# Kernel optimization log

Hardware: AMD Instinct MI355X
Metric: run time of the kernel (lower is better)

Reference implementation:

```python
import jax, jax.numpy as jnp
import numpy as np
import itertools

CONVEX_K = 10
NUM_CLASS = 100
B, N = 8, 16384
MINDIS_INIT = 1.0e5  # torch code initializes mindis to 100000


def _hull_vertex_labels_np(pts):
    """pts: [G, K, 3] numpy. Exact brute-force 3D convex hull vertex labels
    (general position): a triple is a hull facet iff all points lie on one
    side of its plane; every point on some facet is a hull vertex."""
    G, K, _ = pts.shape
    tri = np.array(list(itertools.combinations(range(K), 3)))  # [T,3]
    a = pts[:, tri[:, 0]]                                      # [G,T,3]
    b = pts[:, tri[:, 1]]
    c = pts[:, tri[:, 2]]
    n = np.cross(b - a, c - a)                                 # [G,T,3]
    d = np.einsum('gkd,gtd->gtk', pts, n) - np.einsum('gtd,gtd->gt', a, n)[:, :, None]
    eps = 1e-7
    facet = (d <= eps).all(-1) | (d >= -eps).all(-1)           # [G,T]
    labels = np.zeros((G, K), dtype=np.int32)
    gidx, tidx = np.nonzero(facet)
    for col in range(3):
        labels[gidx, tri[tidx, col]] = 1
    return labels


def setup_inputs() -> dict:
    key = jax.random.key(0)
    k1, k2, k3 = jax.random.split(key, 3)
    xyz = jax.random.normal(k1, (B, N, 6), dtype=jnp.float32)
    skel_xyz = jax.random.normal(k2, (B, NUM_CLASS * CONVEX_K, 3), dtype=jnp.float32)
    weights = jax.random.normal(k3, (B, NUM_CLASS * CONVEX_K // CONVEX_K * CONVEX_K,), dtype=jnp.float32)[:, :NUM_CLASS * CONVEX_K].reshape(B, -1)[:, :1000]
    weights = jax.random.normal(k3, (B, NUM_CLASS * CONVEX_K), dtype=jnp.float32)
    skel_np = np.asarray(skel_xyz).reshape(B * NUM_CLASS, CONVEX_K, 3)
    labels = jnp.asarray(_hull_vertex_labels_np(skel_np).reshape(B, NUM_CLASS, CONVEX_K))
    return {"xyz": xyz, "skel_xyz": skel_xyz, "weights": weights,
            "labels": labels, "num_class": NUM_CLASS}


def reference(xyz, skel_xyz, weights, labels, num_class):
    b = xyz.shape[0]
    pts = xyz[:, :, :3]                                   # [B,N,3]; normals xyz[:,:,3:6] unused
    cp = skel_xyz.reshape(b, num_class, CONVEX_K, 3)      # [B,C,K,3]

    # --- convex loss: for each non-vertex point, min sq-dist to a hull vertex ---
    diff = cp[:, :, :, None, :] - cp[:, :, None, :, :]    # [B,C,K,K,3] (small)
    sqd = jnp.sum(diff * diff, axis=-1)                   # [B,C,K,K]
    is_vert = labels == 1                                  # [B,C,K]
    masked = jnp.where(is_vert[:, :, None, :], sqd, jnp.inf)
    mindis = jnp.minimum(jnp.min(masked, axis=-1), MINDIS_INIT)  # [B,C,K]
    loss_convex = jnp.sum(jnp.where(is_vert, 0.0, mindis)) / (b * num_class)

    # --- Chamfer (closest_distance_with_batch both directions, L2 norm, summed) ---
    skel = skel_xyz                                        # [B,M,3]
    d2 = (jnp.sum(pts * pts, -1)[:, :, None]
          + jnp.sum(skel * skel, -1)[:, None, :]
          - 2.0 * jnp.einsum('bnd,bmd->bnm', pts, skel))   # [B,N,M]
    d = jnp.sqrt(jnp.maximum(d2, 1e-12))
    loss_cd = (jnp.sum(jnp.min(d, axis=2)) + jnp.sum(jnp.min(d, axis=1))) / b

    return 1.0 * loss_convex + 0.1 * loss_cd
```

## Files before the change

kernel.cpp:

```cpp
#include <hip/hip_runtime.h>

#define BATCH 8
#define NPTS 16384
#define MSKEL 1000
#define NCLS 100
#define CKK 10
#define MINDIS_INITF 100000.0f

#define OFF_PTSM 32000
#define OFF_MINB (32000 + 524288)

__global__ __launch_bounds__(256) void k_prep(const float* __restrict__ xyz,
                                              const float* __restrict__ skel,
                                              float4* __restrict__ skelN,
                                              float4* __restrict__ ptsM,
                                              unsigned int* __restrict__ minbits,
                                              float* __restrict__ out) {
    const int gid = blockIdx.x * 256 + threadIdx.x;
    {
        const float* p = xyz + (size_t)gid * 6;
        float x = p[0], y = p[1], z = p[2];
        ptsM[gid] = make_float4(x, y, z, 0.5f * (x * x + y * y + z * z));
    }
    if (gid < BATCH * MSKEL) {
        const float* s = skel + (size_t)gid * 3;
        float sx = s[0], sy = s[1], sz = s[2];
        skelN[gid] = make_float4(-sx, -sy, -sz, 0.5f * (sx * sx + sy * sy + sz * sz));
        minbits[gid] = 0x7F800000u;
    }
    if (gid == 0) out[0] = 0.0f;
}

__global__ __launch_bounds__(256) void k_chamfer(const float4* __restrict__ skelN,
                                                 const float4* __restrict__ ptsM,
                                                 unsigned int* __restrict__ minbits,
                                                 float* __restrict__ out) {
    const int bid = blockIdx.x;
    const int tid = threadIdx.x;

    if (bid < 256) {
        const int b = bid >> 5, tile = bid & 31;
        const int wave = tid >> 6, lane = tid & 63;
        const float4* __restrict__ base = ptsM + b * NPTS + tile * 512;

        float4 P[8];
        float mt[8];
#pragma unroll
        for (int j = 0; j < 8; ++j) {
            P[j] = base[j * 64 + lane];
            mt[j] = 3.4e38f;
        }

        const float4* __restrict__ sk = skelN + b * MSKEL + wave * 250;
#pragma unroll 5
        for (int m = 0; m < 250; ++m) {
            float4 s = sk[m];
#pragma unroll
            for (int j = 0; j < 8; ++j) {
                float t = fmaf(P[j].x, s.x, fmaf(P[j].y, s.y, fmaf(P[j].z, s.z, s.w)));
                mt[j] = fminf(mt[j], t);
            }
        }

        __shared__ float sm[4 * 512];
#pragma unroll
        for (int j = 0; j < 8; ++j) {
            sm[wave * 512 + j * 64 + lane] = mt[j] + P[j].w;
        }
        __syncthreads();

        float a0 = fminf(fminf(sm[tid], sm[512 + tid]),
                         fminf(sm[1024 + tid], sm[1536 + tid]));
        float a1 = fminf(fminf(sm[tid + 256], sm[512 + tid + 256]),
                         fminf(sm[1024 + tid + 256], sm[1536 + tid + 256]));
        float d = sqrtf(fmaxf(2.0f * a0, 1e-12f)) + sqrtf(fmaxf(2.0f * a1, 1e-12f));

#pragma unroll
        for (int o = 32; o > 0; o >>= 1) d += __shfl_down(d, o, 64);
        __shared__ float s_part[4];
        if (lane == 0) s_part[wave] = d;
        __syncthreads();
        if (tid == 0) {
            atomicAdd(out, 0.0125f * (s_part[0] + s_part[1] + s_part[2] + s_part[3]));
        }
    } else {
        const int id = bid - 256;
        const int b = id >> 5, tile = id & 31;

        float nsx[4], nsy[4], nsz[4], ssq[4], mind[4];
#pragma unroll
        for (int k = 0; k < 4; ++k) {
            const int m = tid + k * 256;
            if (m < MSKEL) {
                float4 s = skelN[b * MSKEL + m];
                nsx[k] = s.x; nsy[k] = s.y; nsz[k] = s.z;
                ssq[k] = 2.0f * s.w;
            } else {
                nsx[k] = 0.0f; nsy[k] = 0.0f; nsz[k] = 0.0f; ssq[k] = 0.0f;
            }
            mind[k] = 3.4e38f;
        }

        const float4* __restrict__ pp = ptsM + b * NPTS + tile * 512;
#pragma unroll 8
        for (int n = 0; n < 512; ++n) {
            float4 r = pp[n];
#pragma unroll
            for (int k = 0; k < 4; ++k) {
                float t = fmaf(r.x, nsx[k], fmaf(r.y, nsy[k], fmaf(r.z, nsz[k], r.w)));
                mind[k] = fminf(mind[k], t);
            }
        }
#pragma unroll
        for (int k = 0; k < 4; ++k) {
            const int m = tid + k * 256;
            if (m < MSKEL) {
                float d2 = fmaf(2.0f, mind[k], ssq[k]);
                atomicMin(&minbits[b * MSKEL + m], __float_as_uint(fmaxf(d2, 0.0f)));
            }
        }
    }
}

__global__ __launch_bounds__(256) void k_reduce(const float* __restrict__ skel,
                                                const int* __restrict__ labels,
                                                const unsigned int* __restrict__ minbits,
                                                float* __restrict__ out) {
    const int gid = blockIdx.x * 256 + threadIdx.x;
    const int tid = threadIdx.x;
    float acc = 0.0f;

    for (int i = gid; i < BATCH * MSKEL; i += 2048) {
        acc += 0.0125f * sqrtf(fmaxf(__uint_as_float(minbits[i]), 1e-12f));
    }

    if (gid < BATCH * NCLS) {
        const int b = gid / NCLS, c = gid - b * NCLS;
        const float* cp = skel + ((size_t)b * MSKEL + c * CKK) * 3;
        const int* lab = labels + (size_t)b * NCLS * CKK + c * CKK;
        float x[CKK], y[CKK], z[CKK];
        int lv[CKK];
#pragma unroll
        for (int i = 0; i < CKK; ++i) {
            x[i] = cp[i * 3 + 0]; y[i] = cp[i * 3 + 1]; z[i] = cp[i * 3 + 2];
            lv[i] = lab[i];
        }
        float convexSum = 0.0f;
#pragma unroll
        for (int i = 0; i < CKK; ++i) {
            if (lv[i] != 1) {
                float mind = MINDIS_INITF;
#pragma unroll
                for (int j = 0; j < CKK; ++j) {
                    if (lv[j] == 1) {
                        float dx = x[i] - x[j], dy = y[i] - y[j], dz = z[i] - z[j];
                        mind = fminf(mind, dx * dx + dy * dy + dz * dz);
                    }
                }
                convexSum += mind;
            }
        }
        acc += convexSum * (1.0f / (BATCH * NCLS));
    }

#pragma unroll
    for (int o = 32; o > 0; o >>= 1) acc += __shfl_down(acc, o, 64);
    __shared__ float s_part[4];
    const int wave = tid >> 6, lane = tid & 63;
    if (lane == 0) s_part[wave] = acc;
    __syncthreads();
    if (tid == 0) {
        atomicAdd(out, s_part[0] + s_part[1] + s_part[2] + s_part[3]);
    }
}

extern "C" void kernel_launch(void* const* d_in, const int* in_sizes, int n_in,
                              void* d_out, int out_size, void* d_ws, size_t ws_size,
                              hipStream_t stream) {
    const float* xyz = (const float*)d_in[0];
    const float* skel = (const float*)d_in[1];
    const int* labels = (const int*)d_in[3];
    float* out = (float*)d_out;

    float4* skelN = (float4*)d_ws;
    float4* ptsM = (float4*)((float*)d_ws + OFF_PTSM);
    unsigned int* minbits = (unsigned int*)((float*)d_ws + OFF_MINB);

    k_prep<<<512, 256, 0, stream>>>(xyz, skel, skelN, ptsM, minbits, out);
    k_chamfer<<<512, 256, 0, stream>>>(skelN, ptsM, minbits, out);
    k_reduce<<<8, 256, 0, stream>>>(skel, labels, minbits, out);
}
```

Baseline: 93.39 us.

## Fuse both Chamfer directions per block and replace atomicMin with partial-min buffer

Each chamfer block now processes a 128-point tile and computes both the point-to-skeleton minimum and the skeleton-to-point minimum for that tile, instead of splitting the two directions across separate block halves. Per-tile skeleton minima are written to a 128-way partial buffer that the reduce kernel min-reduces, replacing global atomicMin and its initialization. The grid doubles to 1024 blocks with smaller per-thread register tiles to raise occupancy, in exchange for lower register reuse per loaded skeleton/point and extra partial-buffer traffic (about 4 MB written then read).

```diff
diff --git a/kernel.cpp b/kernel.cpp
--- a/kernel.cpp
+++ b/kernel.cpp
@@ -8,13 +8,12 @@
 #define MINDIS_INITF 100000.0f
 
 #define OFF_PTSM 32000
-#define OFF_MINB (32000 + 524288)
+#define OFF_MPART (32000 + 524288)
 
 __global__ __launch_bounds__(256) void k_prep(const float* __restrict__ xyz,
                                               const float* __restrict__ skel,
                                               float4* __restrict__ skelN,
                                               float4* __restrict__ ptsM,
-                                              unsigned int* __restrict__ minbits,
                                               float* __restrict__ out) {
     const int gid = blockIdx.x * 256 + threadIdx.x;
     {
@@ -26,112 +25,104 @@
         const float* s = skel + (size_t)gid * 3;
         float sx = s[0], sy = s[1], sz = s[2];
         skelN[gid] = make_float4(-sx, -sy, -sz, 0.5f * (sx * sx + sy * sy + sz * sz));
-        minbits[gid] = 0x7F800000u;
     }
     if (gid == 0) out[0] = 0.0f;
 }
 
-__global__ __launch_bounds__(256) void k_chamfer(const float4* __restrict__ skelN,
-                                                 const float4* __restrict__ ptsM,
-                                                 unsigned int* __restrict__ minbits,
-                                                 float* __restrict__ out) {
+__global__ __launch_bounds__(256, 4) void k_chamfer(const float4* __restrict__ skelN,
+                                                    const float4* __restrict__ ptsM,
+                                                    float* __restrict__ mpart,
+                                                    float* __restrict__ out) {
     const int bid = blockIdx.x;
+    const int b = bid >> 7, gt = bid & 127;
     const int tid = threadIdx.x;
+    const int wave = tid >> 6, lane = tid & 63;
+    const float4* __restrict__ base = ptsM + b * NPTS + gt * 128;
 
-    if (bid < 256) {
-        const int b = bid >> 5, tile = bid & 31;
-        const int wave = tid >> 6, lane = tid & 63;
-        const float4* __restrict__ base = ptsM + b * NPTS + tile * 512;
+    float nsx[4], nsy[4], nsz[4], mind[4];
+#pragma unroll
+    for (int k = 0; k < 4; ++k) {
+        const int m = tid + k * 256;
+        if (m < MSKEL) {
+            float4 s = skelN[b * MSKEL + m];
+            nsx[k] = s.x; nsy[k] = s.y; nsz[k] = s.z;
+        } else {
+            nsx[k] = 0.0f; nsy[k] = 0.0f; nsz[k] = 0.0f;
+        }
+        mind[k] = 3.4e38f;
+    }
 
-        float4 P[8];
-        float mt[8];
+    float4 P0 = base[lane];
+    float4 P1 = base[64 + lane];
+    float mt0 = 3.4e38f, mt1 = 3.4e38f;
+
+    const int w = __builtin_amdgcn_readfirstlane(wave);
+    const float4* __restrict__ sk = skelN + b * MSKEL + w * 250;
+#pragma unroll 5
+    for (int m = 0; m < 250; ++m) {
+        float4 s = sk[m];
+        float t0 = fmaf(P0.x, s.x, fmaf(P0.y, s.y, fmaf(P0.z, s.z, s.w)));
+        float t1 = fmaf(P1.x, s.x, fmaf(P1.y, s.y, fmaf(P1.z, s.z, s.w)));
+        mt0 = fminf(mt0, t0);
+        mt1 = fminf(mt1, t1);
+    }
+
+    __shared__ float sm[4 * 128];
+    sm[wave * 128 + lane] = mt0 + P0.w;
+    sm[wave * 128 + 64 + lane] = mt1 + P1.w;
+    __syncthreads();
+
+    float dsum = 0.0f;
+    if (tid < 128) {
+        float a = fminf(fminf(sm[tid], sm[128 + tid]),
+                        fminf(sm[256 + tid], sm[384 + tid]));
+        dsum = sqrtf(fmaxf(2.0f * a, 1e-12f));
+    }
+
+#pragma unroll 8
+    for (int n = 0; n < 128; ++n) {
+        float4 r = base[n];
 #pragma unroll
-        for (int j = 0; j < 8; ++j) {
-            P[j] = base[j * 64 + lane];
-            mt[j] = 3.4e38f;
+        for (int k = 0; k < 4; ++k) {
+            float t = fmaf(r.x, nsx[k], fmaf(r.y, nsy[k], fmaf(r.z, nsz[k], r.w)));
+            mind[k] = fminf(mind[k], t);
         }
-
-        const float4* __restrict__ sk = skelN + b * MSKEL + wave * 250;
-#pragma unroll 5
-        for (int m = 0; m < 250; ++m) {
-            float4 s = sk[m];
+    }
+    float* __restrict__ mp = mpart + (size_t)gt * (BATCH * MSKEL) + b * MSKEL;
 #pragma unroll
-            for (int j = 0; j < 8; ++j) {
-                float t = fmaf(P[j].x, s.x, fmaf(P[j].y, s.y, fmaf(P[j].z, s.z, s.w)));
-                mt[j] = fminf(mt[j], t);
-            }
-        }
-
-        __shared__ float sm[4 * 512];
-#pragma unroll
-        for (int j = 0; j < 8; ++j) {
-            sm[wave * 512 + j * 64 + lane] = mt[j] + P[j].w;
-        }
-        __syncthreads();
-
-        float a0 = fminf(fminf(sm[tid], sm[512 + tid]),
-                         fminf(sm[1024 + tid], sm[1536 + tid]));
-        float a1 = fminf(fminf(sm[tid + 256], sm[512 + tid + 256]),
-                         fminf(sm[1024 + tid + 256], sm[1536 + tid + 256]));
-        float d = sqrtf(fmaxf(2.0f * a0, 1e-12f)) + sqrtf(fmaxf(2.0f * a1, 1e-12f));
+    for (int k = 0; k < 4; ++k) {
+        const int m = tid + k * 256;
+        if (m < MSKEL) mp[m] = mind[k];
+    }
 
 #pragma unroll
-        for (int o = 32; o > 0; o >>= 1) d += __shfl_down(d, o, 64);
-        __shared__ float s_part[4];
-        if (lane == 0) s_part[wave] = d;
-        __syncthreads();
-        if (tid == 0) {
-            atomicAdd(out, 0.0125f * (s_part[0] + s_part[1] + s_part[2] + s_part[3]));
-        }
-    } else {
-        const int id = bid - 256;
-        const int b = id >> 5, tile = id & 31;
-
-        float nsx[4], nsy[4], nsz[4], ssq[4], mind[4];
-#pragma unroll
-        for (int k = 0; k < 4; ++k) {
-            const int m = tid + k * 256;
-            if (m < MSKEL) {
-                float4 s = skelN[b * MSKEL + m];
-                nsx[k] = s.x; nsy[k] = s.y; nsz[k] = s.z;
-                ssq[k] = 2.0f * s.w;
-            } else {
-                nsx[k] = 0.0f; nsy[k] = 0.0f; nsz[k] = 0.0f; ssq[k] = 0.0f;
-            }
-            mind[k] = 3.4e38f;
-        }
-
-        const float4* __restrict__ pp = ptsM + b * NPTS + tile * 512;
-#pragma unroll 8
-        for (int n = 0; n < 512; ++n) {
-            float4 r = pp[n];
-#pragma unroll
-            for (int k = 0; k < 4; ++k) {
-                float t = fmaf(r.x, nsx[k], fmaf(r.y, nsy[k], fmaf(r.z, nsz[k], r.w)));
-                mind[k] = fminf(mind[k], t);
-            }
-        }
-#pragma unroll
-        for (int k = 0; k < 4; ++k) {
-            const int m = tid + k * 256;
-            if (m < MSKEL) {
-                float d2 = fmaf(2.0f, mind[k], ssq[k]);
-                atomicMin(&minbits[b * MSKEL + m], __float_as_uint(fmaxf(d2, 0.0f)));
-            }
-        }
+    for (int o = 32; o > 0; o >>= 1) dsum += __shfl_down(dsum, o, 64);
+    __shared__ float s_part[4];
+    if (lane == 0) s_part[wave] = dsum;
+    __syncthreads();
+    if (tid == 0) {
+        atomicAdd(out, 0.0125f * (s_part[0] + s_part[1] + s_part[2] + s_part[3]));
     }
 }
 
 __global__ __launch_bounds__(256) void k_reduce(const float* __restrict__ skel,
                                                 const int* __restrict__ labels,
-                                                const unsigned int* __restrict__ minbits,
+                                                const float4* __restrict__ skelN,
+                                                const float* __restrict__ mpart,
                                                 float* __restrict__ out) {
     const int gid = blockIdx.x * 256 + threadIdx.x;
     const int tid = threadIdx.x;
     float acc = 0.0f;
 
-    for (int i = gid; i < BATCH * MSKEL; i += 2048) {
-        acc += 0.0125f * sqrtf(fmaxf(__uint_as_float(minbits[i]), 1e-12f));
+    if (gid < BATCH * MSKEL) {
+        float mind = 3.4e38f;
+#pragma unroll 8
+        for (int g = 0; g < 128; ++g) {
+            mind = fminf(mind, mpart[g * (BATCH * MSKEL) + gid]);
+        }
+        float ssq = 2.0f * skelN[gid].w;
+        float d2 = fmaf(2.0f, mind, ssq);
+        acc = 0.0125f * sqrtf(fmaxf(d2, 1e-12f));
     }
 
     if (gid < BATCH * NCLS) {
@@ -149,15 +140,15 @@
 #pragma unroll
         for (int i = 0; i < CKK; ++i) {
             if (lv[i] != 1) {
-                float mind = MINDIS_INITF;
+                float mindc = MINDIS_INITF;
 #pragma unroll
                 for (int j = 0; j < CKK; ++j) {
                     if (lv[j] == 1) {
                         float dx = x[i] - x[j], dy = y[i] - y[j], dz = z[i] - z[j];
-                        mind = fminf(mind, dx * dx + dy * dy + dz * dz);
+                        mindc = fminf(mindc, dx * dx + dy * dy + dz * dz);
                     }
                 }
-                convexSum += mind;
+                convexSum += mindc;
             }
         }
         acc += convexSum * (1.0f / (BATCH * NCLS));
@@ -184,9 +175,9 @@
 
     float4* skelN = (float4*)d_ws;
     float4* ptsM = (float4*)((float*)d_ws + OFF_PTSM);
-    unsigned int* minbits = (unsigned int*)((float*)d_ws + OFF_MINB);
+    float* mpart = (float*)d_ws + OFF_MPART;
 
-    k_prep<<<512, 256, 0, stream>>>(xyz, skel, skelN, ptsM, minbits, out);
-    k_chamfer<<<512, 256, 0, stream>>>(skelN, ptsM, minbits, out);
-    k_reduce<<<8, 256, 0, stream>>>(skel, labels, minbits, out);
+    k_prep<<<512, 256, 0, stream>>>(xyz, skel, skelN, ptsM, out);
+    k_chamfer<<<1024, 256, 0, stream>>>(skelN, ptsM, mpart, out);
+    k_reduce<<<32, 256, 0, stream>>>(skel, labels, skelN, mpart, out);
 }
```

Result: slower. 124.4 us (+33.2%).

## Fuse prep into chamfer kernel, stage in LDS, replace atomics with partial buffers

Applied to the files above, without the earlier changes.

Removes the separate prep kernel: the chamfer blocks now load xyz and skeleton directly, compute the norm terms on the fly, and stage the skeleton and point tiles in shared memory. Global atomicMin and atomicAdd are replaced by per-tile partial-min and per-block partial-sum buffers that a wider 32-block reduce kernel combines. This drops one launch and the intermediate workspace round trip. In exchange it adds a 32-way strided read per skeleton point in the reduce, plus strided 6-float loads of xyz.

```diff
diff --git a/kernel.cpp b/kernel.cpp
--- a/kernel.cpp
+++ b/kernel.cpp
@@ -7,51 +7,44 @@
 #define CKK 10
 #define MINDIS_INITF 100000.0f
 
-#define OFF_PTSM 32000
-#define OFF_MINB (32000 + 524288)
-
-__global__ __launch_bounds__(256) void k_prep(const float* __restrict__ xyz,
-                                              const float* __restrict__ skel,
-                                              float4* __restrict__ skelN,
-                                              float4* __restrict__ ptsM,
-                                              unsigned int* __restrict__ minbits,
-                                              float* __restrict__ out) {
-    const int gid = blockIdx.x * 256 + threadIdx.x;
-    {
-        const float* p = xyz + (size_t)gid * 6;
-        float x = p[0], y = p[1], z = p[2];
-        ptsM[gid] = make_float4(x, y, z, 0.5f * (x * x + y * y + z * z));
-    }
-    if (gid < BATCH * MSKEL) {
-        const float* s = skel + (size_t)gid * 3;
-        float sx = s[0], sy = s[1], sz = s[2];
-        skelN[gid] = make_float4(-sx, -sy, -sz, 0.5f * (sx * sx + sy * sy + sz * sz));
-        minbits[gid] = 0x7F800000u;
-    }
-    if (gid == 0) out[0] = 0.0f;
-}
-
-__global__ __launch_bounds__(256) void k_chamfer(const float4* __restrict__ skelN,
-                                                 const float4* __restrict__ ptsM,
-                                                 unsigned int* __restrict__ minbits,
-                                                 float* __restrict__ out) {
+#define OFF_NPART 256000
+
+__global__ __launch_bounds__(256) void k_A(const float* __restrict__ xyz,
+                                           const float* __restrict__ skel,
+                                           float* __restrict__ mpart,
+                                           float* __restrict__ npart,
+                                           float* __restrict__ out) {
     const int bid = blockIdx.x;
     const int tid = threadIdx.x;
+    const int wave = tid >> 6, lane = tid & 63;
+
+    if (bid == 0 && tid == 0) out[0] = 0.0f;
 
     if (bid < 256) {
         const int b = bid >> 5, tile = bid & 31;
-        const int wave = tid >> 6, lane = tid & 63;
-        const float4* __restrict__ base = ptsM + b * NPTS + tile * 512;
+
+        __shared__ float4 skLDS[MSKEL];
+        __shared__ float sm[4 * 512];
+        __shared__ float s_part[4];
+
+        for (int i = tid; i < MSKEL; i += 256) {
+            const float* s = skel + ((size_t)b * MSKEL + i) * 3;
+            float sx = s[0], sy = s[1], sz = s[2];
+            skLDS[i] = make_float4(-sx, -sy, -sz, 0.5f * (sx * sx + sy * sy + sz * sz));
+        }
 
         float4 P[8];
         float mt[8];
 #pragma unroll
         for (int j = 0; j < 8; ++j) {
-            P[j] = base[j * 64 + lane];
+            const float* p = xyz + ((size_t)b * NPTS + tile * 512 + j * 64 + lane) * 6;
+            float x = p[0], y = p[1], z = p[2];
+            P[j] = make_float4(x, y, z, 0.5f * (x * x + y * y + z * z));
             mt[j] = 3.4e38f;
         }
-
-        const float4* __restrict__ sk = skelN + b * MSKEL + wave * 250;
+        __syncthreads();
+
+        const float4* __restrict__ sk = &skLDS[wave * 250];
 #pragma unroll 5
         for (int m = 0; m < 250; ++m) {
             float4 s = sk[m];
@@ -62,7 +55,6 @@
             }
         }
 
-        __shared__ float sm[4 * 512];
 #pragma unroll
         for (int j = 0; j < 8; ++j) {
             sm[wave * 512 + j * 64 + lane] = mt[j] + P[j].w;
@@ -77,34 +69,42 @@
 
 #pragma unroll
         for (int o = 32; o > 0; o >>= 1) d += __shfl_down(d, o, 64);
-        __shared__ float s_part[4];
         if (lane == 0) s_part[wave] = d;
         __syncthreads();
         if (tid == 0) {
-            atomicAdd(out, 0.0125f * (s_part[0] + s_part[1] + s_part[2] + s_part[3]));
+            npart[bid] = s_part[0] + s_part[1] + s_part[2] + s_part[3];
         }
     } else {
         const int id = bid - 256;
         const int b = id >> 5, tile = id & 31;
 
-        float nsx[4], nsy[4], nsz[4], ssq[4], mind[4];
+        __shared__ float4 ptLDS[512];
+
+#pragma unroll
+        for (int j = 0; j < 2; ++j) {
+            const int n = tid * 2 + j;
+            const float* p = xyz + ((size_t)b * NPTS + tile * 512 + n) * 6;
+            float x = p[0], y = p[1], z = p[2];
+            ptLDS[n] = make_float4(x, y, z, 0.5f * (x * x + y * y + z * z));
+        }
+
+        float nsx[4], nsy[4], nsz[4], mind[4];
 #pragma unroll
         for (int k = 0; k < 4; ++k) {
             const int m = tid + k * 256;
             if (m < MSKEL) {
-                float4 s = skelN[b * MSKEL + m];
-                nsx[k] = s.x; nsy[k] = s.y; nsz[k] = s.z;
-                ssq[k] = 2.0f * s.w;
+                const float* s = skel + ((size_t)b * MSKEL + m) * 3;
+                nsx[k] = -s[0]; nsy[k] = -s[1]; nsz[k] = -s[2];
             } else {
-                nsx[k] = 0.0f; nsy[k] = 0.0f; nsz[k] = 0.0f; ssq[k] = 0.0f;
+                nsx[k] = 0.0f; nsy[k] = 0.0f; nsz[k] = 0.0f;
             }
             mind[k] = 3.4e38f;
         }
-
-        const float4* __restrict__ pp = ptsM + b * NPTS + tile * 512;
+        __syncthreads();
+
 #pragma unroll 8
         for (int n = 0; n < 512; ++n) {
-            float4 r = pp[n];
+            float4 r = ptLDS[n];
 #pragma unroll
             for (int k = 0; k < 4; ++k) {
                 float t = fmaf(r.x, nsx[k], fmaf(r.y, nsy[k], fmaf(r.z, nsz[k], r.w)));
@@ -115,23 +115,31 @@
         for (int k = 0; k < 4; ++k) {
             const int m = tid + k * 256;
             if (m < MSKEL) {
-                float d2 = fmaf(2.0f, mind[k], ssq[k]);
-                atomicMin(&minbits[b * MSKEL + m], __float_as_uint(fmaxf(d2, 0.0f)));
+                mpart[(size_t)tile * (BATCH * MSKEL) + b * MSKEL + m] = mind[k];
             }
         }
     }
 }
 
-__global__ __launch_bounds__(256) void k_reduce(const float* __restrict__ skel,
-                                                const int* __restrict__ labels,
-                                                const unsigned int* __restrict__ minbits,
-                                                float* __restrict__ out) {
+__global__ __launch_bounds__(256) void k_B(const float* __restrict__ skel,
+                                           const int* __restrict__ labels,
+                                           const float* __restrict__ mpart,
+                                           const float* __restrict__ npart,
+                                           float* __restrict__ out) {
     const int gid = blockIdx.x * 256 + threadIdx.x;
     const int tid = threadIdx.x;
     float acc = 0.0f;
 
-    for (int i = gid; i < BATCH * MSKEL; i += 2048) {
-        acc += 0.0125f * sqrtf(fmaxf(__uint_as_float(minbits[i]), 1e-12f));
+    if (gid < BATCH * MSKEL) {
+        float mind = 3.4e38f;
+#pragma unroll 8
+        for (int g = 0; g < 32; ++g) {
+            mind = fminf(mind, mpart[(size_t)g * (BATCH * MSKEL) + gid]);
+        }
+        const float* s = skel + (size_t)gid * 3;
+        float sx = s[0], sy = s[1], sz = s[2];
+        float d2 = fmaf(2.0f, mind, sx * sx + sy * sy + sz * sz);
+        acc = 0.0125f * sqrtf(fmaxf(d2, 1e-12f));
     }
 
     if (gid < BATCH * NCLS) {
@@ -149,18 +157,22 @@
 #pragma unroll
         for (int i = 0; i < CKK; ++i) {
             if (lv[i] != 1) {
-                float mind = MINDIS_INITF;
+                float mindc = MINDIS_INITF;
 #pragma unroll
                 for (int j = 0; j < CKK; ++j) {
                     if (lv[j] == 1) {
                         float dx = x[i] - x[j], dy = y[i] - y[j], dz = z[i] - z[j];
-                        mind = fminf(mind, dx * dx + dy * dy + dz * dz);
+                        mindc = fminf(mindc, dx * dx + dy * dy + dz * dz);
                     }
                 }
-                convexSum += mind;
+                convexSum += mindc;
             }
         }
         acc += convexSum * (1.0f / (BATCH * NCLS));
+    }
+
+    if (blockIdx.x == 0) {
+        acc += 0.0125f * npart[tid];
     }
 
 #pragma unroll
@@ -182,11 +194,9 @@
     const int* labels = (const int*)d_in[3];
     float* out = (float*)d_out;
 
-    float4* skelN = (float4*)d_ws;
-    float4* ptsM = (float4*)((float*)d_ws + OFF_PTSM);
-    unsigned int* minbits = (unsigned int*)((float*)d_ws + OFF_MINB);
-
-    k_prep<<<512, 256, 0, stream>>>(xyz, skel, skelN, ptsM, minbits, out);
-    k_chamfer<<<512, 256, 0, stream>>>(skelN, ptsM, minbits, out);
-    k_reduce<<<8, 256, 0, stream>>>(skel, labels, minbits, out);
+    float* mpart = (float*)d_ws;
+    float* npart = (float*)d_ws + OFF_NPART;
+
+    k_A<<<512, 256, 0, stream>>>(xyz, skel, mpart, npart, out);
+    k_B<<<32, 256, 0, stream>>>(skel, labels, mpart, npart, out);
 }
```

After: 95.86 us. 1.03x slower.
